# Kernel optimization log

Hardware: AMD Instinct MI355X
Metric: run time of the kernel (lower is better)

The kernel has to match this reference:

```python
import jax, jax.numpy as jnp
import numpy as np

B, N, D = 16, 1024, 512
NH = 8
HD = D // NH
K_DEFAULT, K_MAX = 4, 6
PROX_THRESH = 20.0
LN_EPS = 1e-5


def _linear_params(key, din, dout):
    kw, kb = jax.random.split(key)
    lim = 1.0 / np.sqrt(din)
    W = jax.random.uniform(kw, (din, dout), jnp.float32, -lim, lim)
    b = jax.random.uniform(kb, (dout,), jnp.float32, -lim, lim)
    return W, b


def setup_inputs() -> dict:
    key = jax.random.key(0)
    ks = jax.random.split(key, 16)
    agent_repr_1 = jax.random.normal(ks[0], (B, N, D), jnp.float32)
    ego_distance = jax.random.uniform(ks[1], (B, N), jnp.float32) * 100.0  # meters
    ego_mask = jax.random.uniform(ks[2], (B, N), jnp.float32)  # soft ego indicator (torch casts bool->float)
    ego_speed = jax.random.uniform(ks[3], (B,), jnp.float32) * 10.0
    Wq, bq = _linear_params(ks[4], D, D)
    Wk, bk = _linear_params(ks[5], D, D)
    Wv, bv = _linear_params(ks[6], D, D)
    Weq, beq = _linear_params(ks[7], D, D)
    Wek, bek = _linear_params(ks[8], D, D)  # defined in module but unused in forward
    Wev, bev = _linear_params(ks[9], D, D)  # defined in module but unused in forward
    Wd1, bd1 = _linear_params(ks[10], 2, D // 4)
    Wd2, bd2 = _linear_params(ks[11], D // 4, NH)
    ln_g = jnp.ones((D,), jnp.float32)
    ln_b = jnp.zeros((D,), jnp.float32)
    return dict(agent_repr_1=agent_repr_1, ego_distance=ego_distance, ego_mask=ego_mask,
                ego_speed=ego_speed, Wq=Wq, bq=bq, Wk=Wk, bk=bk, Wv=Wv, bv=bv,
                Weq=Weq, beq=beq, Wek=Wek, bek=bek, Wev=Wev, bev=bev,
                Wd1=Wd1, bd1=bd1, Wd2=Wd2, bd2=bd2, ln_g=ln_g, ln_b=ln_b)


def _compute_K(ego_speed, ego_distance):
    # deterministic lookup table; concrete python int (mirrors .item() in torch)
    d = np.asarray(ego_distance)
    s = np.asarray(ego_speed)
    density = (d < PROX_THRESH).astype(np.float32).sum(-1) / max(d.shape[-1], 1)
    K = K_DEFAULT
    if float(s.mean()) > 15.0:
        K = min(K + 1, K_MAX)
    if float(density.mean()) > 0.5:
        K = min(K + 1, K_MAX)
    return K


def _layernorm(x, g, b):
    mu = jnp.mean(x, -1, keepdims=True)
    var = jnp.var(x, -1, keepdims=True)
    return (x - mu) * jax.lax.rsqrt(var + LN_EPS) * g + b


def reference(agent_repr_1, ego_distance, ego_mask, ego_speed,
              Wq, bq, Wk, bk, Wv, bv, Weq, beq, Wek, bek, Wev, bev,
              Wd1, bd1, Wd2, bd2, ln_g, ln_b):
    K = min(_compute_K(ego_speed, ego_distance), N - 1)
    if K <= 0:
        return _layernorm(agent_repr_1, ln_g, ln_b)
    # top-K nearest neighbors by ego distance, excluding self
    dist = jnp.broadcast_to(ego_distance[:, None, :], (B, N, N))  # row i: candidate distances
    dist = jnp.where(jnp.eye(N, dtype=bool)[None], jnp.inf, dist)
    _, topk_idx = jax.lax.top_k(-dist, K)  # [B,N,K] smallest distances
    gathered = jax.vmap(lambda xb, ib: xb[ib])(agent_repr_1, topk_idx)  # [B,N,K,D]
    is_ego = ego_mask[..., None]
    Q = (1.0 - is_ego) * (agent_repr_1 @ Wq + bq) + is_ego * (agent_repr_1 @ Weq + beq)
    Km = gathered @ Wk + bk
    Vm = gathered @ Wv + bv
    Qh = Q.reshape(B, N, NH, HD).transpose(0, 2, 1, 3)          # [B,H,N,hd]
    Kh = Km.reshape(B, N, K, NH, HD).transpose(0, 3, 1, 2, 4)   # [B,H,N,K,hd]
    Vh = Vm.reshape(B, N, K, NH, HD).transpose(0, 3, 1, 2, 4)
    scores = jnp.einsum('bhnd,bhnkd->bhnk', Qh, Kh) / np.sqrt(HD)
    q_dist = jnp.broadcast_to(ego_distance[:, :, None], (B, N, K))
    k_dist = jnp.take_along_axis(jnp.broadcast_to(ego_distance[:, None, :], (B, N, N)), topk_idx, axis=2)
    dist_pair = jnp.stack([q_dist, k_dist], -1)                 # [B,N,K,2]
    bias = jax.nn.relu(dist_pair @ Wd1 + bd1) @ Wd2 + bd2       # [B,N,K,H]
    scores = scores * bias.transpose(0, 3, 1, 2)                # multiplicative distance bias
    attn = jax.nn.softmax(scores, axis=-1)
    attn_out = jnp.einsum('bhnk,bhnkd->bhnd', attn, Vh)
    attn_out = attn_out.transpose(0, 2, 1, 3).reshape(B, N, D)
    return _layernorm(agent_repr_1 + attn_out, ln_g, ln_b)
```

## Files before the change

### kernel.cpp

```cpp
#include <hip/hip_runtime.h>
#include <math.h>

constexpr int CB  = 16;
constexpr int CN  = 1024;
constexpr int CD  = 512;
constexpr int KM1 = 7;
constexpr int RB  = 32;

typedef __attribute__((ext_vector_type(8))) short bf8;
typedef __attribute__((ext_vector_type(4))) float f32x4;
typedef __attribute__((ext_vector_type(4))) unsigned short us4;

__device__ inline float bf2f(unsigned short u) {
    union { unsigned int i; float f; } v; v.i = ((unsigned)u) << 16; return v.f;
}
__device__ inline unsigned short f2bf(float f) {
    union { unsigned int i; float f; } v; v.f = f;
    unsigned r = v.i + 0x7FFFu + ((v.i >> 16) & 1u);
    return (unsigned short)(r >> 16);
}
__device__ inline unsigned int cvtpk(float lo, float hi) {
    unsigned int r;
    asm("v_cvt_pk_bf16_f32 %0, %1, %2" : "=v"(r) : "v"(lo), "v"(hi));
    return r;
}
__device__ inline bf8 pack8(float4 x, float4 y) {
    union { bf8 v; unsigned int u[4]; } r;
    r.u[0] = cvtpk(x.x, x.y); r.u[1] = cvtpk(x.z, x.w);
    r.u[2] = cvtpk(y.x, y.y); r.u[3] = cvtpk(y.z, y.w);
    return r.v;
}
__device__ inline us4 pack4(float4 x) {
    union { us4 v; unsigned int u[2]; } r;
    r.u[0] = cvtpk(x.x, x.y); r.u[1] = cvtpk(x.z, x.w);
    return r.v;
}

__global__ __launch_bounds__(256) void k_pre(
    const float* __restrict__ dist, const float* __restrict__ speed,
    const float* __restrict__ Wk, const float* __restrict__ Wv,
    int* __restrict__ Kout,
    int* __restrict__ candIdx, float* __restrict__ candDist,
    unsigned short* __restrict__ WkT, unsigned short* __restrict__ WvT) {
    int t = threadIdx.x;
    int bid = blockIdx.x;

    if (bid < 16) {
        __shared__ float sdist[CN];
        __shared__ unsigned long long red64[4];
        int b = bid;
        for (int i = t; i < CN; i += 256) sdist[i] = dist[b * CN + i];
        __syncthreads();
        for (int sel = 0; sel < KM1; sel++) {
            unsigned long long best = 0xFFFFFFFFFFFFFFFFull;
            for (int i = t; i < CN; i += 256) {
                unsigned long long key =
                    ((unsigned long long)__float_as_uint(sdist[i]) << 32) | (unsigned)i;
                best = best < key ? best : key;
            }
#pragma unroll
            for (int off = 32; off; off >>= 1) {
                unsigned long long o = __shfl_xor(best, off);
                best = best < o ? best : o;
            }
            if ((t & 63) == 0) red64[t >> 6] = best;
            __syncthreads();
            if (t == 0) {
                unsigned long long m0 = red64[0] < red64[1] ? red64[0] : red64[1];
                unsigned long long m1 = red64[2] < red64[3] ? red64[2] : red64[3];
                unsigned long long m = m0 < m1 ? m0 : m1;
                int idx = (int)(unsigned)(m & 0xFFFFFFFFu);
                candIdx[b * KM1 + sel]  = idx;
                candDist[b * KM1 + sel] = __uint_as_float((unsigned)(m >> 32));
                sdist[idx] = 3.4e38f;
            }
            __syncthreads();
        }
        return;
    }
    if (bid < 144) {
        __shared__ unsigned short tile[64][68];
        int b2 = bid - 16;
        int kt = b2 & 7, ct = (b2 >> 3) & 7, mat = b2 >> 6;
        const float* W = mat ? Wv : Wk;
        unsigned short* WT = mat ? WvT : WkT;
        int k0 = kt * 64, c0 = ct * 64;
#pragma unroll
        for (int p = 0; p < 4; p++) {
            int kr = p * 16 + (t >> 4);
            int cc = (t & 15) * 4;
            float4 v = *(const float4*)(W + (size_t)(k0 + kr) * CD + c0 + cc);
            *(us4*)&tile[kr][cc] = pack4(v);
        }
        __syncthreads();
#pragma unroll
        for (int p = 0; p < 4; p++) {
            int cr = p * 16 + (t >> 4);
            int kk = (t & 15) * 4;
            us4 o;
            o.x = tile[kk + 0][cr];
            o.y = tile[kk + 1][cr];
            o.z = tile[kk + 2][cr];
            o.w = tile[kk + 3][cr];
            *(us4*)(WT + (size_t)(c0 + cr) * CD + k0 + kk) = o;
        }
        return;
    }
    {
        __shared__ int red[256];
        int cnt = 0;
        for (int i = t; i < CB * CN; i += 256) cnt += (dist[i] < 20.0f) ? 1 : 0;
        red[t] = cnt;
        __syncthreads();
        for (int s = 128; s > 0; s >>= 1) {
            if (t < s) red[t] += red[t + s];
            __syncthreads();
        }
        if (t == 0) {
            float ss = 0.f;
            for (int i = 0; i < CB; i++) ss += speed[i];
            int K = 4;
            if (ss / (float)CB > 15.0f) K = (K + 1 > 6) ? 6 : K + 1;
            float density = (float)red[0] / (float)(CB * CN);
            if (density > 0.5f) K = (K + 1 > 6) ? 6 : K + 1;
            if (K > CN - 1) K = CN - 1;
            if (K < 0) K = 0;
            *Kout = K;
        }
    }
}

__global__ __launch_bounds__(256) void k_mid(
    const float* __restrict__ X,
    const unsigned short* __restrict__ WkT, const float* __restrict__ bk,
    const unsigned short* __restrict__ WvT, const float* __restrict__ bv,
    const float* __restrict__ Wq, const float* __restrict__ bq,
    const float* __restrict__ Weq, const float* __restrict__ beq,
    const int* __restrict__ candIdx,
    unsigned short* __restrict__ VcB, float* __restrict__ S0,
    unsigned short* __restrict__ Y,
    unsigned short* __restrict__ X2) {
    int t = threadIdx.x;
    int bid = blockIdx.x;
    __shared__ unsigned short sbuf[RB][520];

    if (bid >= 384) {
        int tileId = bid - 384;
        int b = tileId >> 5, rblk = tileId & 31;
        int row0 = b * CN + rblk * RB;
        for (int idx = t; idx < RB * 128; idx += 256) {
            int r = idx >> 7, c4 = idx & 127;
            float4 xv = *(const float4*)(X + (size_t)(row0 + r) * CD + c4 * 4);
            *(us4*)&sbuf[r][c4 * 4] = pack4(xv);
        }
        __syncthreads();
        unsigned short* dst = X2 + (size_t)tileId * 16384;
#pragma unroll
        for (int it = 0; it < 8; it++) {
            int unit = t + it * 256;
            int r = unit & 31, kg = (unit >> 5) & 3, s = unit >> 7;
            const unsigned short* src = &sbuf[r][s * 32 + kg * 8];
            us4 lo = *(const us4*)src;
            us4 hi = *(const us4*)(src + 4);
            *(us4*)(dst + (size_t)unit * 8)     = lo;
            *(us4*)(dst + (size_t)unit * 8 + 4) = hi;
        }
        return;
    }

    int b = (bid < 128) ? (bid >> 3) : ((bid - 128) >> 4);
    for (int i = t; i < 16 * 128; i += 256) {
        int m = i >> 7, c4 = i & 127;
        float4 xv = {0.f, 0.f, 0.f, 0.f};
        if (m < KM1)
            xv = *(const float4*)(X + (size_t)(b * CN + candIdx[b * KM1 + m]) * CD + c4 * 4);
        *(us4*)&sbuf[m][c4 * 4] = pack4(xv);
    }
    __syncthreads();

    int w = t >> 6, lane = t & 63, lr = lane & 15, kg = lane >> 4;

    if (bid < 128) {
        int ny = bid & 7;
        int c = ny * 64 + w * 16 + lr;
        const unsigned short* wtp = WvT + (size_t)c * CD + kg * 8;
        f32x4 acc = {0.f, 0.f, 0.f, 0.f};
#pragma unroll
        for (int s = 0; s < 16; s++) {
            bf8 bfr = *(const bf8*)(wtp + s * 32);
            bf8 a   = *(const bf8*)&sbuf[lr][s * 32 + kg * 8];
            acc = __builtin_amdgcn_mfma_f32_16x16x32_bf16(a, bfr, acc, 0, 0, 0);
        }
        float bv_ = bv[c];
#pragma unroll
        for (int q = 0; q < 4; q++) {
            int m = kg * 4 + q;
            if (m < KM1)
                VcB[(size_t)(b * KM1 + m) * CD + c] = f2bf(acc[q] + bv_);
        }
        return;
    }

    int rem = (bid - 128) & 15;
    int h = rem >> 1, half = rem & 1;
    __shared__ unsigned short sKc16[16][68];
    __shared__ float sKcf[KM1][64];

    {
        int c = h * 64 + w * 16 + lr;
        const unsigned short* wtp = WkT + (size_t)c * CD + kg * 8;
        f32x4 acc = {0.f, 0.f, 0.f, 0.f};
#pragma unroll
        for (int s = 0; s < 16; s++) {
            bf8 bfr = *(const bf8*)(wtp + s * 32);
            bf8 a   = *(const bf8*)&sbuf[lr][s * 32 + kg * 8];
            acc = __builtin_amdgcn_mfma_f32_16x16x32_bf16(a, bfr, acc, 0, 0, 0);
        }
        float bk_ = bk[c];
        int cl = w * 16 + lr;
#pragma unroll
        for (int q = 0; q < 4; q++) {
            int m = kg * 4 + q;
            float val = (m < KM1) ? (acc[q] + bk_) : 0.f;
            sKc16[m][cl] = f2bf(val);
            if (m < KM1) sKcf[m][cl] = val;
        }
    }
    __syncthreads();

    if (half == 0 && t < 14) {
        int mat = t / 7, m = t % 7;
        const float* bias = mat ? beq : bq;
        float s = 0.f;
        for (int c = 0; c < 64; c++) s = fmaf(bias[h * 64 + c], sKcf[m][c], s);
        S0[((b * 2 + mat) * KM1 + m) * 8 + h] = s;
    }

    bf8 a0 = *(const bf8*)&sKc16[lr][kg * 8];
    bf8 a1 = *(const bf8*)&sKc16[lr][32 + kg * 8];
    unsigned short* Y2b = Y + (size_t)b * 64 * 112 * 8;
#pragma unroll
    for (int mat = 0; mat < 2; mat++) {
        const float* W = mat ? Weq : Wq;
#pragma unroll
        for (int nt = 0; nt < 4; nt++) {
            int n0 = (half * 16 + w * 4 + nt) * 16;
            const float* wp = W + (size_t)(n0 + lr) * CD + h * 64 + kg * 8;
            float4 f0 = *(const float4*)(wp);
            float4 f1 = *(const float4*)(wp + 4);
            float4 f2 = *(const float4*)(wp + 32);
            float4 f3 = *(const float4*)(wp + 36);
            f32x4 acc = {0.f, 0.f, 0.f, 0.f};
            acc = __builtin_amdgcn_mfma_f32_16x16x32_bf16(a0, pack8(f0, f1), acc, 0, 0, 0);
            acc = __builtin_amdgcn_mfma_f32_16x16x32_bf16(a1, pack8(f2, f3), acc, 0, 0, 0);
            int k_out = n0 + lr;
            int k8 = k_out >> 3, krem = k_out & 7;
#pragma unroll
            for (int q = 0; q < 4; q++) {
                int m = kg * 4 + q;
                if (m < KM1) {
                    int n = mat * 56 + m * 8 + h;
                    Y2b[((size_t)k8 * 112 + n) * 8 + krem] = f2bf(acc[q]);
                }
            }
        }
    }
}

__global__ __launch_bounds__(512) void k_attn(
    const float* __restrict__ X, const float* __restrict__ dist,
    const float* __restrict__ mask,
    const float* __restrict__ Wd1, const float* __restrict__ bd1,
    const float* __restrict__ Wd2, const float* __restrict__ bd2,
    const float* __restrict__ lng, const float* __restrict__ lnb,
    const int* __restrict__ Kp, const int* __restrict__ candIdx,
    const float* __restrict__ candDist,
    const unsigned short* __restrict__ VcB, const float* __restrict__ S0,
    const unsigned short* __restrict__ Y,
    const unsigned short* __restrict__ X2, int useX2,
    float* __restrict__ out) {

    __shared__ float sS[RB][116];
    __shared__ unsigned short sVc[KM1][520];
    __shared__ float sW7[RB][8][8];
    __shared__ float sBias[RB][6][2][8];
    __shared__ int   snbr[RB][6];
    __shared__ float skd[RB][6];
    __shared__ float srd[RB];
    __shared__ float sE[RB];
    __shared__ float sS0[112];

    int t = threadIdx.x;
    int b = blockIdx.x >> 5, rblk = blockIdx.x & 31;
    int row0 = b * CN + rblk * RB;
    int K = *Kp;

    for (int idx = t; idx < KM1 * 128; idx += 512) {
        int m = idx >> 7, c4 = idx & 127;
        *(us4*)&sVc[m][c4 * 4] =
            *(const us4*)(VcB + (size_t)(b * KM1 + m) * CD + c4 * 4);
    }
    if (t < 112) sS0[t] = S0[b * 112 + t];
    if (t < RB) {
        int i = rblk * RB + t;
        sE[t]  = mask[b * CN + i];
        srd[t] = dist[b * CN + i];
        int cnt = 0;
        for (int m = 0; m <= K && cnt < K; m++) {
            int c = candIdx[b * KM1 + m];
            if (c != i) { snbr[t][cnt] = m; skd[t][cnt] = candDist[b * KM1 + m]; cnt++; }
        }
    }
    __syncthreads();

    int w = t >> 6;
    if (w < 4) {
        int lane = t & 63, lr = lane & 15, kg = lane >> 4;
        f32x4 acc00 = {0.f, 0.f, 0.f, 0.f}, acc10 = acc00, acc01 = acc00, acc11 = acc00;
        bool has2 = (w < 3);
        const unsigned short* ypk = Y + ((size_t)b * 64 * 112 + (size_t)kg * 112 + (w * 16 + lr)) * 8;
        if (useX2) {
            const unsigned short* x2s = X2 + (size_t)blockIdx.x * 16384 + kg * 256 + lr * 8;
#pragma unroll
            for (int s = 0; s < 16; s++) {
                const unsigned short* xp = x2s + s * 1024;
                bf8 a0 = *(const bf8*)xp;
                bf8 a1 = *(const bf8*)(xp + 128);
                const unsigned short* ys = ypk + (size_t)s * 4 * 112 * 8;
                bf8 b0 = *(const bf8*)ys;
                acc00 = __builtin_amdgcn_mfma_f32_16x16x32_bf16(a0, b0, acc00, 0, 0, 0);
                acc10 = __builtin_amdgcn_mfma_f32_16x16x32_bf16(a1, b0, acc10, 0, 0, 0);
                if (has2) {
                    bf8 b1 = *(const bf8*)(ys + 512);
                    acc01 = __builtin_amdgcn_mfma_f32_16x16x32_bf16(a0, b1, acc01, 0, 0, 0);
                    acc11 = __builtin_amdgcn_mfma_f32_16x16x32_bf16(a1, b1, acc11, 0, 0, 0);
                }
            }
        } else {
            const float* x0 = X + (size_t)(row0 + lr) * CD + kg * 8;
            const float* x1 = X + (size_t)(row0 + 16 + lr) * CD + kg * 8;
#pragma unroll
            for (int s = 0; s < 16; s++) {
                int k0 = s * 32;
                float4 xa0 = *(const float4*)(x0 + k0);
                float4 xb0 = *(const float4*)(x0 + k0 + 4);
                float4 xa1 = *(const float4*)(x1 + k0);
                float4 xb1 = *(const float4*)(x1 + k0 + 4);
                bf8 a0 = pack8(xa0, xb0);
                bf8 a1 = pack8(xa1, xb1);
                const unsigned short* ys = ypk + (size_t)s * 4 * 112 * 8;
                bf8 b0 = *(const bf8*)ys;
                acc00 = __builtin_amdgcn_mfma_f32_16x16x32_bf16(a0, b0, acc00, 0, 0, 0);
                acc10 = __builtin_amdgcn_mfma_f32_16x16x32_bf16(a1, b0, acc10, 0, 0, 0);
                if (has2) {
                    bf8 b1 = *(const bf8*)(ys + 512);
                    acc01 = __builtin_amdgcn_mfma_f32_16x16x32_bf16(a0, b1, acc01, 0, 0, 0);
                    acc11 = __builtin_amdgcn_mfma_f32_16x16x32_bf16(a1, b1, acc11, 0, 0, 0);
                }
            }
        }
        int n0 = w * 16 + lr;
#pragma unroll
        for (int q = 0; q < 4; q++) {
            sS[kg * 4 + q][n0]      = acc00[q];
            sS[16 + kg * 4 + q][n0] = acc10[q];
        }
        if (has2) {
            int n1 = (w + 4) * 16 + lr;
#pragma unroll
            for (int q = 0; q < 4; q++) {
                sS[kg * 4 + q][n1]      = acc01[q];
                sS[16 + kg * 4 + q][n1] = acc11[q];
            }
        }
    } else {
        int tot2 = RB * K * 2;
        for (int task = t - 256; task < tot2; task += 256) {
            int half = task & 1;
            int pid = task >> 1;
            int r = pid / K, k = pid - r * K;
            int j0 = half * 64;
            float qd = srd[r], kd = skd[r][k];
            float bacc[8];
#pragma unroll
            for (int h = 0; h < 8; h++) bacc[h] = 0.f;
            for (int j = j0; j < j0 + 64; j++) {
                float hid = fmaf(qd, Wd1[j], fmaf(kd, Wd1[128 + j], bd1[j]));
                hid = fmaxf(hid, 0.f);
                float4 wa = *(const float4*)(Wd2 + j * 8);
                float4 wb = *(const float4*)(Wd2 + j * 8 + 4);
                bacc[0] = fmaf(hid, wa.x, bacc[0]);
                bacc[1] = fmaf(hid, wa.y, bacc[1]);
                bacc[2] = fmaf(hid, wa.z, bacc[2]);
                bacc[3] = fmaf(hid, wa.w, bacc[3]);
                bacc[4] = fmaf(hid, wb.x, bacc[4]);
                bacc[5] = fmaf(hid, wb.y, bacc[5]);
                bacc[6] = fmaf(hid, wb.z, bacc[6]);
                bacc[7] = fmaf(hid, wb.w, bacc[7]);
            }
#pragma unroll
            for (int h = 0; h < 8; h++) sBias[r][k][half][h] = bacc[h];
        }
    }
    __syncthreads();

    if (t < RB * 8) {
        int r = t >> 3, h = t & 7;
        float e = sE[r];
        float wv[6];
#pragma unroll
        for (int k = 0; k < 6; k++) {
            if (k < K) {
                int m = snbr[r][k];
                float scq = sS[r][m * 8 + h]      + sS0[m * 8 + h];
                float sce = sS[r][56 + m * 8 + h] + sS0[56 + m * 8 + h];
                float sc = (1.f - e) * scq + e * sce;
                float bias = sBias[r][k][0][h] + sBias[r][k][1][h] + bd2[h];
                wv[k] = sc * 0.125f * bias;
            } else {
                wv[k] = -3.4e38f;
            }
        }
        float mx = -3.4e38f;
#pragma unroll
        for (int k = 0; k < 6; k++) mx = fmaxf(mx, wv[k]);
        float sum = 0.f;
#pragma unroll
        for (int k = 0; k < 6; k++) {
            wv[k] = __expf(wv[k] - mx);
            sum += wv[k];
        }
        float inv = 1.f / sum;
#pragma unroll
        for (int m = 0; m < KM1; m++) {
            float acc = 0.f;
#pragma unroll
            for (int k = 0; k < 6; k++) {
                bool use = (k < K) && (snbr[r][k] == m);
                acc += use ? wv[k] * inv : 0.f;
            }
            sW7[r][h][m] = acc;
        }
    }
    __syncthreads();

    {
        int r = t >> 4, tr = t & 15;
        const float* xrow = X + (size_t)(row0 + r) * CD;
        float4 vals[8];
        float sum = 0.f, sq = 0.f;
#pragma unroll
        for (int j = 0; j < 8; j++) {
            int d = tr * 4 + j * 64;
            float ax = 0.f, ay = 0.f, az = 0.f, aw = 0.f;
#pragma unroll
            for (int m = 0; m < KM1; m++) {
                float wgt = sW7[r][j][m];
                us4 vv = *(const us4*)&sVc[m][d];
                ax = fmaf(wgt, bf2f(vv.x), ax);
                ay = fmaf(wgt, bf2f(vv.y), ay);
                az = fmaf(wgt, bf2f(vv.z), az);
                aw = fmaf(wgt, bf2f(vv.w), aw);
            }
            float4 xv = *(const float4*)(xrow + d);
            float4 v;
            v.x = xv.x + ax; v.y = xv.y + ay; v.z = xv.z + az; v.w = xv.w + aw;
            vals[j] = v;
            sum += v.x + v.y + v.z + v.w;
            sq = fmaf(v.x, v.x, sq); sq = fmaf(v.y, v.y, sq);
            sq = fmaf(v.z, v.z, sq); sq = fmaf(v.w, v.w, sq);
        }
        sum += __shfl_xor(sum, 1, 16); sq += __shfl_xor(sq, 1, 16);
        sum += __shfl_xor(sum, 2, 16); sq += __shfl_xor(sq, 2, 16);
        sum += __shfl_xor(sum, 4, 16); sq += __shfl_xor(sq, 4, 16);
        sum += __shfl_xor(sum, 8, 16); sq += __shfl_xor(sq, 8, 16);
        float mu  = sum * (1.f / 512.f);
        float var = sq * (1.f / 512.f) - mu * mu;
        float inv = rsqrtf(var + 1e-5f);
        float* orow = out + (size_t)(row0 + r) * CD;
#pragma unroll
        for (int j = 0; j < 8; j++) {
            int d = tr * 4 + j * 64;
            float4 g  = *(const float4*)(lng + d);
            float4 bb = *(const float4*)(lnb + d);
            float4 v = vals[j];
            float4 o;
            o.x = (v.x - mu) * inv * g.x + bb.x;
            o.y = (v.y - mu) * inv * g.y + bb.y;
            o.z = (v.z - mu) * inv * g.z + bb.z;
            o.w = (v.w - mu) * inv * g.w + bb.w;
            *(float4*)(orow + d) = o;
        }
    }
}

extern "C" void kernel_launch(void* const* d_in, const int* in_sizes, int n_in,
                              void* d_out, int out_size, void* d_ws, size_t ws_size,
                              hipStream_t stream) {
    (void)in_sizes; (void)n_in; (void)out_size;
    const float* X     = (const float*)d_in[0];
    const float* dist  = (const float*)d_in[1];
    const float* mask  = (const float*)d_in[2];
    const float* speed = (const float*)d_in[3];
    const float* Wq    = (const float*)d_in[4];
    const float* bq    = (const float*)d_in[5];
    const float* Wk    = (const float*)d_in[6];
    const float* bk    = (const float*)d_in[7];
    const float* Wv    = (const float*)d_in[8];
    const float* bv    = (const float*)d_in[9];
    const float* Weq   = (const float*)d_in[10];
    const float* beq   = (const float*)d_in[11];
    const float* Wd1   = (const float*)d_in[16];
    const float* bd1   = (const float*)d_in[17];
    const float* Wd2   = (const float*)d_in[18];
    const float* bd2   = (const float*)d_in[19];
    const float* lng   = (const float*)d_in[20];
    const float* lnb   = (const float*)d_in[21];
    float* out = (float*)d_out;

    char* ws = (char*)d_ws;
    int*   Kp       = (int*)(ws);
    int*   candIdx  = (int*)(ws + 256);
    float* candDist = (float*)(ws + 1024);
    float* S0       = (float*)(ws + 2048);
    unsigned short* VcB = (unsigned short*)(ws + 245760);
    unsigned short* Y   = (unsigned short*)(ws + 475136);
    unsigned short* WkT = (unsigned short*)(ws + 2310144);
    unsigned short* WvT = (unsigned short*)(ws + 2834432);
    unsigned short* X2  = (unsigned short*)(ws + 3358720);
    int useX2 = (ws_size >= (size_t)3358720 + 16777216) ? 1 : 0;

    k_pre<<<145, 256, 0, stream>>>(dist, speed, Wk, Wv, Kp, candIdx, candDist, WkT, WvT);
    int midBlocks = 384 + (useX2 ? 512 : 0);
    k_mid<<<midBlocks, 256, 0, stream>>>(X, WkT, bk, WvT, bv, Wq, bq, Weq, beq,
                                         candIdx, VcB, S0, Y, X2);
    k_attn<<<CB * (CN / RB), 512, 0, stream>>>(X, dist, mask, Wd1, bd1, Wd2, bd2, lng, lnb,
                                               Kp, candIdx, candDist, VcB, S0, Y,
                                               X2, useX2, out);
}
```

Baseline: 71.82 us.

## Stage X tile in shared memory as bf16 inside attention kernel, drop X2 pre-pass

Removes the k_mid pre-pass that repacked X into a bf16 X2 buffer in global memory. k_attn now loads its 32-row X tile once into LDS as bf16 and reuses it for both the MFMA A-operands and the residual add before layernorm. This saves a global write and re-read of X2 plus one extra fp32 read of X. The cost is more LDS per block, which may lower occupancy, and the residual now uses bf16-rounded X instead of fp32, which loses some precision.

```diff
diff --git a/kernel.cpp b/kernel.cpp
--- a/kernel.cpp
+++ b/kernel.cpp
@@ -138,35 +138,10 @@
     const float* __restrict__ Weq, const float* __restrict__ beq,
     const int* __restrict__ candIdx,
     unsigned short* __restrict__ VcB, float* __restrict__ S0,
-    unsigned short* __restrict__ Y,
-    unsigned short* __restrict__ X2) {
+    unsigned short* __restrict__ Y) {
     int t = threadIdx.x;
     int bid = blockIdx.x;
-    __shared__ unsigned short sbuf[RB][520];
-
-    if (bid >= 384) {
-        int tileId = bid - 384;
-        int b = tileId >> 5, rblk = tileId & 31;
-        int row0 = b * CN + rblk * RB;
-        for (int idx = t; idx < RB * 128; idx += 256) {
-            int r = idx >> 7, c4 = idx & 127;
-            float4 xv = *(const float4*)(X + (size_t)(row0 + r) * CD + c4 * 4);
-            *(us4*)&sbuf[r][c4 * 4] = pack4(xv);
-        }
-        __syncthreads();
-        unsigned short* dst = X2 + (size_t)tileId * 16384;
-#pragma unroll
-        for (int it = 0; it < 8; it++) {
-            int unit = t + it * 256;
-            int r = unit & 31, kg = (unit >> 5) & 3, s = unit >> 7;
-            const unsigned short* src = &sbuf[r][s * 32 + kg * 8];
-            us4 lo = *(const us4*)src;
-            us4 hi = *(const us4*)(src + 4);
-            *(us4*)(dst + (size_t)unit * 8)     = lo;
-            *(us4*)(dst + (size_t)unit * 8 + 4) = hi;
-        }
-        return;
-    }
+    __shared__ unsigned short sbuf[16][520];
 
     int b = (bid < 128) ? (bid >> 3) : ((bid - 128) >> 4);
     for (int i = t; i < 16 * 128; i += 256) {
@@ -277,9 +252,9 @@
     const float* __restrict__ candDist,
     const unsigned short* __restrict__ VcB, const float* __restrict__ S0,
     const unsigned short* __restrict__ Y,
-    const unsigned short* __restrict__ X2, int useX2,
     float* __restrict__ out) {
 
+    __shared__ unsigned short sX[RB][520];
     __shared__ float sS[RB][116];
     __shared__ unsigned short sVc[KM1][520];
     __shared__ float sW7[RB][8][8];
@@ -295,6 +270,11 @@
     int row0 = b * CN + rblk * RB;
     int K = *Kp;
 
+    for (int idx = t; idx < RB * 128; idx += 512) {
+        int r = idx >> 7, c4 = idx & 127;
+        float4 xv = *(const float4*)(X + (size_t)(row0 + r) * CD + c4 * 4);
+        *(us4*)&sX[r][c4 * 4] = pack4(xv);
+    }
     for (int idx = t; idx < KM1 * 128; idx += 512) {
         int m = idx >> 7, c4 = idx & 127;
         *(us4*)&sVc[m][c4 * 4] =
@@ -319,44 +299,19 @@
         f32x4 acc00 = {0.f, 0.f, 0.f, 0.f}, acc10 = acc00, acc01 = acc00, acc11 = acc00;
         bool has2 = (w < 3);
         const unsigned short* ypk = Y + ((size_t)b * 64 * 112 + (size_t)kg * 112 + (w * 16 + lr)) * 8;
-        if (useX2) {
-            const unsigned short* x2s = X2 + (size_t)blockIdx.x * 16384 + kg * 256 + lr * 8;
-#pragma unroll
-            for (int s = 0; s < 16; s++) {
-                const unsigned short* xp = x2s + s * 1024;
-                bf8 a0 = *(const bf8*)xp;
-                bf8 a1 = *(const bf8*)(xp + 128);
-                const unsigned short* ys = ypk + (size_t)s * 4 * 112 * 8;
-                bf8 b0 = *(const bf8*)ys;
-                acc00 = __builtin_amdgcn_mfma_f32_16x16x32_bf16(a0, b0, acc00, 0, 0, 0);
-                acc10 = __builtin_amdgcn_mfma_f32_16x16x32_bf16(a1, b0, acc10, 0, 0, 0);
-                if (has2) {
-                    bf8 b1 = *(const bf8*)(ys + 512);
-                    acc01 = __builtin_amdgcn_mfma_f32_16x16x32_bf16(a0, b1, acc01, 0, 0, 0);
-                    acc11 = __builtin_amdgcn_mfma_f32_16x16x32_bf16(a1, b1, acc11, 0, 0, 0);
-                }
-            }
-        } else {
-            const float* x0 = X + (size_t)(row0 + lr) * CD + kg * 8;
-            const float* x1 = X + (size_t)(row0 + 16 + lr) * CD + kg * 8;
-#pragma unroll
-            for (int s = 0; s < 16; s++) {
-                int k0 = s * 32;
-                float4 xa0 = *(const float4*)(x0 + k0);
-                float4 xb0 = *(const float4*)(x0 + k0 + 4);
-                float4 xa1 = *(const float4*)(x1 + k0);
-                float4 xb1 = *(const float4*)(x1 + k0 + 4);
-                bf8 a0 = pack8(xa0, xb0);
-                bf8 a1 = pack8(xa1, xb1);
-                const unsigned short* ys = ypk + (size_t)s * 4 * 112 * 8;
-                bf8 b0 = *(const bf8*)ys;
-                acc00 = __builtin_amdgcn_mfma_f32_16x16x32_bf16(a0, b0, acc00, 0, 0, 0);
-                acc10 = __builtin_amdgcn_mfma_f32_16x16x32_bf16(a1, b0, acc10, 0, 0, 0);
-                if (has2) {
-                    bf8 b1 = *(const bf8*)(ys + 512);
-                    acc01 = __builtin_amdgcn_mfma_f32_16x16x32_bf16(a0, b1, acc01, 0, 0, 0);
-                    acc11 = __builtin_amdgcn_mfma_f32_16x16x32_bf16(a1, b1, acc11, 0, 0, 0);
-                }
+#pragma unroll
+        for (int s = 0; s < 16; s++) {
+            int k0 = s * 32 + kg * 8;
+            bf8 a0 = *(const bf8*)&sX[lr][k0];
+            bf8 a1 = *(const bf8*)&sX[16 + lr][k0];
+            const unsigned short* ys = ypk + (size_t)s * 4 * 112 * 8;
+            bf8 b0 = *(const bf8*)ys;
+            acc00 = __builtin_amdgcn_mfma_f32_16x16x32_bf16(a0, b0, acc00, 0, 0, 0);
+            acc10 = __builtin_amdgcn_mfma_f32_16x16x32_bf16(a1, b0, acc10, 0, 0, 0);
+            if (has2) {
+                bf8 b1 = *(const bf8*)(ys + 512);
+                acc01 = __builtin_amdgcn_mfma_f32_16x16x32_bf16(a0, b1, acc01, 0, 0, 0);
+                acc11 = __builtin_amdgcn_mfma_f32_16x16x32_bf16(a1, b1, acc11, 0, 0, 0);
             }
         }
         int n0 = w * 16 + lr;
@@ -446,7 +401,6 @@
 
     {
         int r = t >> 4, tr = t & 15;
-        const float* xrow = X + (size_t)(row0 + r) * CD;
         float4 vals[8];
         float sum = 0.f, sq = 0.f;
 #pragma unroll
@@ -462,9 +416,10 @@
                 az = fmaf(wgt, bf2f(vv.z), az);
                 aw = fmaf(wgt, bf2f(vv.w), aw);
             }
-            float4 xv = *(const float4*)(xrow + d);
+            us4 xb = *(const us4*)&sX[r][d];
             float4 v;
-            v.x = xv.x + ax; v.y = xv.y + ay; v.z = xv.z + az; v.w = xv.w + aw;
+            v.x = bf2f(xb.x) + ax; v.y = bf2f(xb.y) + ay;
+            v.z = bf2f(xb.z) + az; v.w = bf2f(xb.w) + aw;
             vals[j] = v;
             sum += v.x + v.y + v.z + v.w;
             sq = fmaf(v.x, v.x, sq); sq = fmaf(v.y, v.y, sq);
@@ -477,7 +432,8 @@
         float mu  = sum * (1.f / 512.f);
         float var = sq * (1.f / 512.f) - mu * mu;
         float inv = rsqrtf(var + 1e-5f);
-        float* orow = out + (size_t)(row0 + r) * CD;
+        int gr = row0 + r;
+        float* orow = out + (size_t)gr * CD;
 #pragma unroll
         for (int j = 0; j < 8; j++) {
             int d = tr * 4 + j * 64;
@@ -497,7 +453,7 @@
 extern "C" void kernel_launch(void* const* d_in, const int* in_sizes, int n_in,
                               void* d_out, int out_size, void* d_ws, size_t ws_size,
                               hipStream_t stream) {
-    (void)in_sizes; (void)n_in; (void)out_size;
+    (void)in_sizes; (void)n_in; (void)out_size; (void)ws_size;
     const float* X     = (const float*)d_in[0];
     const float* dist  = (const float*)d_in[1];
     const float* mask  = (const float*)d_in[2];
@@ -527,14 +483,10 @@
     unsigned short* Y   = (unsigned short*)(ws + 475136);
     unsigned short* WkT = (unsigned short*)(ws + 2310144);
     unsigned short* WvT = (unsigned short*)(ws + 2834432);
-    unsigned short* X2  = (unsigned short*)(ws + 3358720);
-    int useX2 = (ws_size >= (size_t)3358720 + 16777216) ? 1 : 0;
 
     k_pre<<<145, 256, 0, stream>>>(dist, speed, Wk, Wv, Kp, candIdx, candDist, WkT, WvT);
-    int midBlocks = 384 + (useX2 ? 512 : 0);
-    k_mid<<<midBlocks, 256, 0, stream>>>(X, WkT, bk, WvT, bv, Wq, bq, Weq, beq,
-                                         candIdx, VcB, S0, Y, X2);
+    k_mid<<<384, 256, 0, stream>>>(X, WkT, bk, WvT, bv, Wq, bq, Weq, beq,
+                                   candIdx, VcB, S0, Y);
     k_attn<<<CB * (CN / RB), 512, 0, stream>>>(X, dist, mask, Wd1, bd1, Wd2, bd2, lng, lnb,
-                                               Kp, candIdx, candDist, VcB, S0, Y,
-                                               X2, useX2, out);
-}
+                                               Kp, candIdx, candDist, VcB, S0, Y, out);
+}
```

Measured after the change: 80.88 us. 1.13x slower.
